# Kernel optimization log

Hardware: AMD Instinct MI355X
Metric: run time of the kernel (lower is better)

The kernel has to match this reference:

```python
import jax, jax.numpy as jnp
import numpy as np

SIZE = 2.0            # scene extent, matches init size
N_LEVELS = 16         # Instant-NGP default
TABLE_SIZE = 1 << 19  # hash entries per level (power of 2)
FEAT = 2              # embedding_length per level
BASE_RES = 16         # init resolution
MAX_RES = 2048
N_POINTS = 1 << 21

_OFFS = np.array([[(c >> d) & 1 for d in range(3)] for c in range(8)])  # [8,3] corner bits
_PRIMES = np.array([1, 2654435761, 805459861], dtype=np.uint32)         # NGP spatial hash primes


def setup_inputs() -> dict:
    key = jax.random.key(0)
    k1, k2 = jax.random.split(key)
    xyz = (jax.random.uniform(k1, (N_POINTS, 3), dtype=jnp.float32) - 0.5) * SIZE
    tables = jax.random.normal(k2, (N_LEVELS, TABLE_SIZE, FEAT), dtype=jnp.float32) * 1e-2
    # geometric resolution schedule 16 -> 2048 over 16 levels
    growth = (MAX_RES / BASE_RES) ** (np.arange(N_LEVELS) / (N_LEVELS - 1))
    resolutions = jnp.asarray(np.floor(BASE_RES * growth).astype(np.int32))
    return {"xyz": xyz, "tables": tables, "resolutions": resolutions}


def _encode(xyz, tables, resolutions):
    u = xyz / SIZE + 0.5                              # [N,3] in [0,1)
    offs_u = jnp.asarray(_OFFS.astype(np.uint32))     # [8,3]
    offs_f = jnp.asarray(_OFFS.astype(np.float32))    # [8,3]
    primes = jnp.asarray(_PRIMES)

    def level(_, xs):
        table, res = xs                               # [T,F], scalar int32
        p = u * res.astype(jnp.float32)               # [N,3]
        p0 = jnp.floor(p)
        w = p - p0                                    # trilinear fractions [N,3]
        c = p0.astype(jnp.uint32)[:, None, :] + offs_u[None]     # [N,8,3]
        h = (c[..., 0] * primes[0]) ^ (c[..., 1] * primes[1]) ^ (c[..., 2] * primes[2])
        idx = (h & jnp.uint32(TABLE_SIZE - 1)).astype(jnp.int32)  # [N,8]
        feats = table[idx]                                        # [N,8,F] gather
        wc = jnp.prod(jnp.where(offs_f[None] > 0, w[:, None, :], 1.0 - w[:, None, :]), axis=-1)  # [N,8]
        return None, jnp.sum(feats * wc[..., None], axis=1)      # [N,F]

    _, embs = jax.lax.scan(level, None, (tables, resolutions))   # [L,N,F]
    n = xyz.shape[0]
    return jnp.transpose(embs, (1, 0, 2)).reshape(n, N_LEVELS * FEAT)


def reference(xyz, tables, resolutions):
    return _encode(xyz, tables, resolutions)
```

## Files before the change

### kernel.cpp

```cpp
#include <hip/hip_runtime.h>
#include <hip/hip_fp16.h>

#define NLV 16
#define TBL (1u << 19)
#define TMASK (TBL - 1u)
#define P1 2654435761u
#define P2 805459861u

typedef float vf2 __attribute__((ext_vector_type(2)));
typedef float vf4 __attribute__((ext_vector_type(4)));
typedef unsigned vu2 __attribute__((ext_vector_type(2)));
typedef unsigned vu4 __attribute__((ext_vector_type(4)));

__device__ __forceinline__ vf2 h2_to_f2(unsigned bits) {
    union { unsigned u; __half2 h; } c; c.u = bits;
    float2 f = __half22float2(c.h);
    vf2 r; r.x = f.x; r.y = f.y; return r;
}
__device__ __forceinline__ unsigned f2_to_h2(float a, float b) {
    union { __half2 h; unsigned u; } c; c.h = __floats2half2_rn(a, b);
    return c.u;
}

__global__ __launch_bounds__(256) void convert_tables(
    const float* __restrict__ tables, unsigned* __restrict__ htab, int total)
{
    int i = blockIdx.x * 256 + threadIdx.x;
    int e0 = i * 2;
    if (e0 >= total) return;
    vf4 v = *(const vf4*)(tables + (size_t)e0 * 2);
    vu2 o; o.x = f2_to_h2(v.x, v.y); o.y = f2_to_h2(v.z, v.w);
    *(vu2*)(htab + e0) = o;
}

__global__ __launch_bounds__(256) void pack_u4(
    const float* __restrict__ xyz, vf4* __restrict__ u4, int n)
{
    int p = blockIdx.x * 256 + threadIdx.x;
    if (p >= n) return;
    float x = xyz[(size_t)p * 3 + 0];
    float y = xyz[(size_t)p * 3 + 1];
    float z = xyz[(size_t)p * 3 + 2];
    vf4 r; r.x = x * 0.5f + 0.5f; r.y = y * 0.5f + 0.5f;
    r.z = z * 0.5f + 0.5f; r.w = 0.0f;
    u4[p] = r;
}

__global__ __launch_bounds__(256) void ngp_gather_h(
    const vf4* __restrict__ u4,
    const unsigned* __restrict__ htab,
    const int* __restrict__ resolutions,
    unsigned* __restrict__ wsout,
    int n, int nbPerLevel)
{
    int L = blockIdx.x / nbPerLevel;
    int chunk = blockIdx.x % nbPerLevel;
    int p0 = chunk * 1024 + (int)threadIdx.x;

    float res = (float)resolutions[L];
    const unsigned* __restrict__ tab = htab + (size_t)L * TBL;
    unsigned* __restrict__ wl = wsout + (size_t)L * n;

    unsigned Rj[4][4];
    unsigned e[4], odd[4];
    float wx[4], wyz[4][4];
    bool valid[4];

#pragma unroll
    for (int q = 0; q < 4; ++q) {
        int p = p0 + q * 256;
        valid[q] = (p < n);
        int pp = valid[q] ? p : 0;
        vf4 u = u4[pp];
        float px = u.x * res, py = u.y * res, pz = u.z * res;
        float fx = floorf(px), fy = floorf(py), fz = floorf(pz);
        float wxl = px - fx, wyl = py - fy, wzl = pz - fz;
        unsigned cx = (unsigned)fx, cy = (unsigned)fy, cz = (unsigned)fz;
        e[q] = cx & ~1u;
        odd[q] = cx & 1u;
        unsigned hy0 = cy * P1, hy1 = hy0 + P1;
        unsigned hz0 = cz * P2, hz1 = hz0 + P2;
        Rj[q][0] = hy0 ^ hz0; Rj[q][1] = hy1 ^ hz0;
        Rj[q][2] = hy0 ^ hz1; Rj[q][3] = hy1 ^ hz1;
        float vy = 1.0f - wyl, vz = 1.0f - wzl;
        wx[q] = wxl;
        wyz[q][0] = vy * vz; wyz[q][1] = wyl * vz;
        wyz[q][2] = vy * wzl; wyz[q][3] = wyl * wzl;
    }

    vu2 dA[4][4];
#pragma unroll
    for (int q = 0; q < 4; ++q)
#pragma unroll
        for (int j = 0; j < 4; ++j) {
            unsigned idx = (e[q] ^ Rj[q][j]) & TMASK;
            dA[q][j] = *(const vu2*)(tab + (idx & ~1u));
        }

    vu2 dB[4][4];
#pragma unroll
    for (int q = 0; q < 4; ++q) {
#pragma unroll
        for (int j = 0; j < 4; ++j) { dB[q][j].x = 0u; dB[q][j].y = 0u; }
        if (odd[q]) {
#pragma unroll
            for (int j = 0; j < 4; ++j) {
                unsigned idx = ((e[q] + 2u) ^ Rj[q][j]) & TMASK;
                dB[q][j] = *(const vu2*)(tab + (idx & ~1u));
            }
        }
    }

#pragma unroll
    for (int q = 0; q < 4; ++q) {
        float vx = 1.0f - wx[q];
        float a0 = 0.0f, a1 = 0.0f;
#pragma unroll
        for (int j = 0; j < 4; ++j) {
            unsigned sA = Rj[q][j] & 1u;
            unsigned s0 = sA ^ odd[q];
            unsigned b0 = s0 ? dA[q][j].y : dA[q][j].x;
            unsigned fromA = sA ? dA[q][j].x : dA[q][j].y;
            unsigned fromB = sA ? dB[q][j].y : dB[q][j].x;
            unsigned b1 = odd[q] ? fromB : fromA;
            vf2 f0 = h2_to_f2(b0);
            vf2 f1 = h2_to_f2(b1);
            float W0 = wyz[q][j] * vx;
            float W1 = wyz[q][j] * wx[q];
            a0 += f0.x * W0; a0 += f1.x * W1;
            a1 += f0.y * W0; a1 += f1.y * W1;
        }
        int p = p0 + q * 256;
        if (valid[q]) wl[p] = f2_to_h2(a0, a1);
    }
}

__global__ __launch_bounds__(256) void ngp_transpose_h(
    const unsigned* __restrict__ ws,
    float* __restrict__ out, int n)
{
    int t = blockIdx.x * 256 + threadIdx.x;
    int p = t * 4;
    if (p >= n) return;

    if (p + 3 < n && (n & 3) == 0) {
        vu4 m[NLV];
#pragma unroll
        for (int L = 0; L < NLV; ++L)
            m[L] = *(const vu4*)(ws + (size_t)L * n + p);
#pragma unroll
        for (int pt = 0; pt < 4; ++pt) {
            vf4* o = (vf4*)(out + (size_t)(p + pt) * (NLV * 2));
#pragma unroll
            for (int i = 0; i < 8; ++i) {
                unsigned ba = pt == 0 ? m[2 * i].x : pt == 1 ? m[2 * i].y
                             : pt == 2 ? m[2 * i].z : m[2 * i].w;
                unsigned bb = pt == 0 ? m[2 * i + 1].x : pt == 1 ? m[2 * i + 1].y
                             : pt == 2 ? m[2 * i + 1].z : m[2 * i + 1].w;
                vf2 ga = h2_to_f2(ba), gb = h2_to_f2(bb);
                vf4 r; r.x = ga.x; r.y = ga.y; r.z = gb.x; r.w = gb.y;
                o[i] = r;
            }
        }
    } else {
        for (int pt = 0; pt < 4 && p + pt < n; ++pt) {
            vf4* o = (vf4*)(out + (size_t)(p + pt) * (NLV * 2));
#pragma unroll
            for (int i = 0; i < 8; ++i) {
                vf2 ga = h2_to_f2(ws[(size_t)(2 * i) * n + p + pt]);
                vf2 gb = h2_to_f2(ws[(size_t)(2 * i + 1) * n + p + pt]);
                vf4 r; r.x = ga.x; r.y = ga.y; r.z = gb.x; r.w = gb.y;
                o[i] = r;
            }
        }
    }
}

__global__ __launch_bounds__(256) void ngp_encode_kernel(
    const float* __restrict__ xyz,
    const float* __restrict__ tables,
    const int* __restrict__ resolutions,
    float* __restrict__ out,
    int n)
{
    int p = blockIdx.x * blockDim.x + threadIdx.x;
    if (p >= n) return;

    float x = xyz[(size_t)p * 3 + 0];
    float y = xyz[(size_t)p * 3 + 1];
    float z = xyz[(size_t)p * 3 + 2];
    float ux = x * 0.5f + 0.5f;
    float uy = y * 0.5f + 0.5f;
    float uz = z * 0.5f + 0.5f;

    float acc[NLV * 2];

#pragma unroll
    for (int L = 0; L < NLV; ++L) {
        float res = (float)resolutions[L];
        float px = ux * res, py = uy * res, pz = uz * res;
        float fx = floorf(px), fy = floorf(py), fz = floorf(pz);
        float wx = px - fx, wy = py - fy, wz = pz - fz;
        unsigned cx = (unsigned)fx, cy = (unsigned)fy, cz = (unsigned)fz;
        unsigned hx0 = cx, hx1 = cx + 1u;
        unsigned hy0 = cy * P1, hy1 = hy0 + P1;
        unsigned hz0 = cz * P2, hz1 = hz0 + P2;
        const vf2* __restrict__ tab = (const vf2*)tables + (size_t)L * TBL;
        float vx = 1.0f - wx, vy = 1.0f - wy, vz = 1.0f - wz;
        float a0 = 0.0f, a1 = 0.0f;
#pragma unroll
        for (int c = 0; c < 8; ++c) {
            unsigned h = ((c & 1) ? hx1 : hx0) ^
                         ((c & 2) ? hy1 : hy0) ^
                         ((c & 4) ? hz1 : hz0);
            vf2 f = tab[h & TMASK];
            float w = ((c & 1) ? wx : vx) *
                      ((c & 2) ? wy : vy) *
                      ((c & 4) ? wz : vz);
            a0 += f.x * w;
            a1 += f.y * w;
        }
        acc[L * 2 + 0] = a0;
        acc[L * 2 + 1] = a1;
    }

    vf4* o = (vf4*)(out + (size_t)p * (NLV * 2));
#pragma unroll
    for (int i = 0; i < 8; ++i) {
        vf4 r; r.x = acc[i * 4 + 0]; r.y = acc[i * 4 + 1];
        r.z = acc[i * 4 + 2]; r.w = acc[i * 4 + 3];
        o[i] = r;
    }
}

extern "C" void kernel_launch(void* const* d_in, const int* in_sizes, int n_in,
                              void* d_out, int out_size, void* d_ws, size_t ws_size,
                              hipStream_t stream) {
    const float* xyz = (const float*)d_in[0];
    const float* tables = (const float*)d_in[1];
    const int* resolutions = (const int*)d_in[2];
    float* out = (float*)d_out;

    int n = in_sizes[0] / 3;
    const int totalEntries = NLV * (int)TBL;
    const size_t tabBytes = (size_t)totalEntries * 4;
    const size_t u4Bytes = (size_t)n * sizeof(vf4);
    const size_t wsoutBytes = (size_t)NLV * (size_t)n * 4;

    if (ws_size >= tabBytes + u4Bytes + wsoutBytes) {
        unsigned* htab = (unsigned*)d_ws;
        vf4* u4 = (vf4*)((char*)d_ws + tabBytes);
        unsigned* wsout = (unsigned*)((char*)d_ws + tabBytes + u4Bytes);

        int gridC = (totalEntries / 2 + 255) / 256;
        hipLaunchKernelGGL(convert_tables, dim3(gridC), dim3(256), 0, stream,
                           tables, htab, totalEntries);

        int gridU = (n + 255) / 256;
        hipLaunchKernelGGL(pack_u4, dim3(gridU), dim3(256), 0, stream,
                           xyz, u4, n);

        int nbPerLevel = (n + 1023) / 1024;
        int grid1 = NLV * nbPerLevel;
        hipLaunchKernelGGL(ngp_gather_h, dim3(grid1), dim3(256), 0, stream,
                           u4, htab, resolutions, wsout, n, nbPerLevel);

        int grid2 = ((n + 3) / 4 + 255) / 256;
        hipLaunchKernelGGL(ngp_transpose_h, dim3(grid2), dim3(256), 0, stream,
                           wsout, out, n);
    } else {
        int grid = (n + 255) / 256;
        hipLaunchKernelGGL(ngp_encode_kernel, dim3(grid), dim3(256), 0, stream,
                           xyz, tables, resolutions, out, n);
    }
}
```

Baseline: 898.4 us.

## Sort points into Morton-ordered spatial bins before hash-grid gather

Adds a counting sort of points into 2^18 Morton-ordered spatial bins (histogram, single-block scan, atomic scatter), so the gather kernel processes spatially nearby points together and gets better cache locality in the hash tables. The gather now does eight plain 4-byte loads per point instead of the paired-entry trick, and the final kernel scatters rows back to original order through an index array. This costs three extra passes over the points, many atomics, and a serial one-block scan, and the final output writes become non-contiguous.

```diff
diff --git a/kernel.cpp b/kernel.cpp
--- a/kernel.cpp
+++ b/kernel.cpp
@@ -6,11 +6,11 @@
 #define TMASK (TBL - 1u)
 #define P1 2654435761u
 #define P2 805459861u
+#define NBIN (1 << 18)
 
 typedef float vf2 __attribute__((ext_vector_type(2)));
 typedef float vf4 __attribute__((ext_vector_type(4)));
 typedef unsigned vu2 __attribute__((ext_vector_type(2)));
-typedef unsigned vu4 __attribute__((ext_vector_type(4)));
 
 __device__ __forceinline__ vf2 h2_to_f2(unsigned bits) {
     union { unsigned u; __half2 h; } c; c.u = bits;
@@ -20,6 +20,22 @@
 __device__ __forceinline__ unsigned f2_to_h2(float a, float b) {
     union { __half2 h; unsigned u; } c; c.h = __floats2half2_rn(a, b);
     return c.u;
+}
+
+__device__ __forceinline__ unsigned mort6(unsigned v) {
+    v &= 63u;
+    v = (v | (v << 16)) & 0x030000FFu;
+    v = (v | (v << 8))  & 0x0300F00Fu;
+    v = (v | (v << 4))  & 0x030C30C3u;
+    v = (v | (v << 2))  & 0x09249249u;
+    return v;
+}
+
+__device__ __forceinline__ unsigned bin_of(float ux, float uy, float uz) {
+    unsigned bx = min(63u, (unsigned)(ux * 64.0f));
+    unsigned by = min(63u, (unsigned)(uy * 64.0f));
+    unsigned bz = min(63u, (unsigned)(uz * 64.0f));
+    return mort6(bx) | (mort6(by) << 1) | (mort6(bz) << 2);
 }
 
 __global__ __launch_bounds__(256) void convert_tables(
@@ -33,21 +49,57 @@
     *(vu2*)(htab + e0) = o;
 }
 
-__global__ __launch_bounds__(256) void pack_u4(
-    const float* __restrict__ xyz, vf4* __restrict__ u4, int n)
+__global__ __launch_bounds__(256) void hist_kernel(
+    const float* __restrict__ xyz, unsigned* __restrict__ hist, int n)
 {
     int p = blockIdx.x * 256 + threadIdx.x;
     if (p >= n) return;
-    float x = xyz[(size_t)p * 3 + 0];
-    float y = xyz[(size_t)p * 3 + 1];
-    float z = xyz[(size_t)p * 3 + 2];
-    vf4 r; r.x = x * 0.5f + 0.5f; r.y = y * 0.5f + 0.5f;
-    r.z = z * 0.5f + 0.5f; r.w = 0.0f;
-    u4[p] = r;
-}
-
-__global__ __launch_bounds__(256) void ngp_gather_h(
-    const vf4* __restrict__ u4,
+    float ux = xyz[(size_t)p * 3 + 0] * 0.5f + 0.5f;
+    float uy = xyz[(size_t)p * 3 + 1] * 0.5f + 0.5f;
+    float uz = xyz[(size_t)p * 3 + 2] * 0.5f + 0.5f;
+    atomicAdd(&hist[bin_of(ux, uy, uz)], 1u);
+}
+
+__global__ __launch_bounds__(1024) void scan_bins(unsigned* __restrict__ hist)
+{
+    __shared__ unsigned part[1024];
+    int t = threadIdx.x;
+    int base = t * (NBIN / 1024);
+    unsigned s = 0;
+    for (int j = 0; j < NBIN / 1024; ++j) s += hist[base + j];
+    part[t] = s;
+    __syncthreads();
+    for (int off = 1; off < 1024; off <<= 1) {
+        unsigned v = (t >= off) ? part[t - off] : 0u;
+        __syncthreads();
+        part[t] += v;
+        __syncthreads();
+    }
+    unsigned run = (t == 0) ? 0u : part[t - 1];
+    for (int j = 0; j < NBIN / 1024; ++j) {
+        unsigned tmp = hist[base + j];
+        hist[base + j] = run;
+        run += tmp;
+    }
+}
+
+__global__ __launch_bounds__(256) void scatter_kernel(
+    const float* __restrict__ xyz, unsigned* __restrict__ start,
+    vf4* __restrict__ u4s, int* __restrict__ orig, int n)
+{
+    int p = blockIdx.x * 256 + threadIdx.x;
+    if (p >= n) return;
+    float ux = xyz[(size_t)p * 3 + 0] * 0.5f + 0.5f;
+    float uy = xyz[(size_t)p * 3 + 1] * 0.5f + 0.5f;
+    float uz = xyz[(size_t)p * 3 + 2] * 0.5f + 0.5f;
+    unsigned pos = atomicAdd(&start[bin_of(ux, uy, uz)], 1u);
+    orig[pos] = p;
+    vf4 r; r.x = ux; r.y = uy; r.z = uz; r.w = 0.0f;
+    u4s[pos] = r;
+}
+
+__global__ __launch_bounds__(256) void ngp_gather_s(
+    const vf4* __restrict__ u4s,
     const unsigned* __restrict__ htab,
     const int* __restrict__ resolutions,
     unsigned* __restrict__ wsout,
@@ -61,8 +113,7 @@
     const unsigned* __restrict__ tab = htab + (size_t)L * TBL;
     unsigned* __restrict__ wl = wsout + (size_t)L * n;
 
-    unsigned Rj[4][4];
-    unsigned e[4], odd[4];
+    unsigned idx[4][8];
     float wx[4], wyz[4][4];
     bool valid[4];
 
@@ -71,108 +122,62 @@
         int p = p0 + q * 256;
         valid[q] = (p < n);
         int pp = valid[q] ? p : 0;
-        vf4 u = u4[pp];
+        vf4 u = u4s[pp];
         float px = u.x * res, py = u.y * res, pz = u.z * res;
         float fx = floorf(px), fy = floorf(py), fz = floorf(pz);
         float wxl = px - fx, wyl = py - fy, wzl = pz - fz;
         unsigned cx = (unsigned)fx, cy = (unsigned)fy, cz = (unsigned)fz;
-        e[q] = cx & ~1u;
-        odd[q] = cx & 1u;
+        unsigned hx0 = cx, hx1 = cx + 1u;
         unsigned hy0 = cy * P1, hy1 = hy0 + P1;
         unsigned hz0 = cz * P2, hz1 = hz0 + P2;
-        Rj[q][0] = hy0 ^ hz0; Rj[q][1] = hy1 ^ hz0;
-        Rj[q][2] = hy0 ^ hz1; Rj[q][3] = hy1 ^ hz1;
+#pragma unroll
+        for (int c = 0; c < 8; ++c)
+            idx[q][c] = ((((c & 1) ? hx1 : hx0) ^
+                          ((c & 2) ? hy1 : hy0) ^
+                          ((c & 4) ? hz1 : hz0)) & TMASK);
         float vy = 1.0f - wyl, vz = 1.0f - wzl;
         wx[q] = wxl;
-        wyz[q][0] = vy * vz; wyz[q][1] = wyl * vz;
+        wyz[q][0] = vy * vz;  wyz[q][1] = wyl * vz;
         wyz[q][2] = vy * wzl; wyz[q][3] = wyl * wzl;
     }
 
-    vu2 dA[4][4];
+    unsigned d[4][8];
 #pragma unroll
     for (int q = 0; q < 4; ++q)
 #pragma unroll
-        for (int j = 0; j < 4; ++j) {
-            unsigned idx = (e[q] ^ Rj[q][j]) & TMASK;
-            dA[q][j] = *(const vu2*)(tab + (idx & ~1u));
-        }
-
-    vu2 dB[4][4];
-#pragma unroll
-    for (int q = 0; q < 4; ++q) {
-#pragma unroll
-        for (int j = 0; j < 4; ++j) { dB[q][j].x = 0u; dB[q][j].y = 0u; }
-        if (odd[q]) {
-#pragma unroll
-            for (int j = 0; j < 4; ++j) {
-                unsigned idx = ((e[q] + 2u) ^ Rj[q][j]) & TMASK;
-                dB[q][j] = *(const vu2*)(tab + (idx & ~1u));
-            }
-        }
-    }
+        for (int c = 0; c < 8; ++c)
+            d[q][c] = tab[idx[q][c]];
 
 #pragma unroll
     for (int q = 0; q < 4; ++q) {
         float vx = 1.0f - wx[q];
         float a0 = 0.0f, a1 = 0.0f;
 #pragma unroll
-        for (int j = 0; j < 4; ++j) {
-            unsigned sA = Rj[q][j] & 1u;
-            unsigned s0 = sA ^ odd[q];
-            unsigned b0 = s0 ? dA[q][j].y : dA[q][j].x;
-            unsigned fromA = sA ? dA[q][j].x : dA[q][j].y;
-            unsigned fromB = sA ? dB[q][j].y : dB[q][j].x;
-            unsigned b1 = odd[q] ? fromB : fromA;
-            vf2 f0 = h2_to_f2(b0);
-            vf2 f1 = h2_to_f2(b1);
-            float W0 = wyz[q][j] * vx;
-            float W1 = wyz[q][j] * wx[q];
-            a0 += f0.x * W0; a0 += f1.x * W1;
-            a1 += f0.y * W0; a1 += f1.y * W1;
+        for (int c = 0; c < 8; ++c) {
+            float w = wyz[q][c >> 1] * ((c & 1) ? wx[q] : vx);
+            vf2 f = h2_to_f2(d[q][c]);
+            a0 += f.x * w;
+            a1 += f.y * w;
         }
         int p = p0 + q * 256;
         if (valid[q]) wl[p] = f2_to_h2(a0, a1);
     }
 }
 
-__global__ __launch_bounds__(256) void ngp_transpose_h(
-    const unsigned* __restrict__ ws,
+__global__ __launch_bounds__(256) void ngp_finalize_s(
+    const unsigned* __restrict__ ws, const int* __restrict__ orig,
     float* __restrict__ out, int n)
 {
-    int t = blockIdx.x * 256 + threadIdx.x;
-    int p = t * 4;
-    if (p >= n) return;
-
-    if (p + 3 < n && (n & 3) == 0) {
-        vu4 m[NLV];
-#pragma unroll
-        for (int L = 0; L < NLV; ++L)
-            m[L] = *(const vu4*)(ws + (size_t)L * n + p);
-#pragma unroll
-        for (int pt = 0; pt < 4; ++pt) {
-            vf4* o = (vf4*)(out + (size_t)(p + pt) * (NLV * 2));
-#pragma unroll
-            for (int i = 0; i < 8; ++i) {
-                unsigned ba = pt == 0 ? m[2 * i].x : pt == 1 ? m[2 * i].y
-                             : pt == 2 ? m[2 * i].z : m[2 * i].w;
-                unsigned bb = pt == 0 ? m[2 * i + 1].x : pt == 1 ? m[2 * i + 1].y
-                             : pt == 2 ? m[2 * i + 1].z : m[2 * i + 1].w;
-                vf2 ga = h2_to_f2(ba), gb = h2_to_f2(bb);
-                vf4 r; r.x = ga.x; r.y = ga.y; r.z = gb.x; r.w = gb.y;
-                o[i] = r;
-            }
-        }
-    } else {
-        for (int pt = 0; pt < 4 && p + pt < n; ++pt) {
-            vf4* o = (vf4*)(out + (size_t)(p + pt) * (NLV * 2));
-#pragma unroll
-            for (int i = 0; i < 8; ++i) {
-                vf2 ga = h2_to_f2(ws[(size_t)(2 * i) * n + p + pt]);
-                vf2 gb = h2_to_f2(ws[(size_t)(2 * i + 1) * n + p + pt]);
-                vf4 r; r.x = ga.x; r.y = ga.y; r.z = gb.x; r.w = gb.y;
-                o[i] = r;
-            }
-        }
+    int i = blockIdx.x * 256 + threadIdx.x;
+    if (i >= n) return;
+    int op = orig[i];
+    vf4* o = (vf4*)(out + (size_t)op * (NLV * 2));
+#pragma unroll
+    for (int j = 0; j < 8; ++j) {
+        vf2 ga = h2_to_f2(ws[(size_t)(2 * j) * n + i]);
+        vf2 gb = h2_to_f2(ws[(size_t)(2 * j + 1) * n + i]);
+        vf4 r; r.x = ga.x; r.y = ga.y; r.z = gb.x; r.w = gb.y;
+        o[j] = r;
     }
 }
 
@@ -243,31 +248,42 @@
 
     int n = in_sizes[0] / 3;
     const int totalEntries = NLV * (int)TBL;
-    const size_t tabBytes = (size_t)totalEntries * 4;
-    const size_t u4Bytes = (size_t)n * sizeof(vf4);
+
+    const size_t tabBytes  = (size_t)totalEntries * 4;
+    const size_t u4Bytes   = (size_t)n * sizeof(vf4);
+    const size_t origBytes = (size_t)n * 4;
+    const size_t histBytes = (size_t)NBIN * 4;
     const size_t wsoutBytes = (size_t)NLV * (size_t)n * 4;
-
-    if (ws_size >= tabBytes + u4Bytes + wsoutBytes) {
-        unsigned* htab = (unsigned*)d_ws;
-        vf4* u4 = (vf4*)((char*)d_ws + tabBytes);
-        unsigned* wsout = (unsigned*)((char*)d_ws + tabBytes + u4Bytes);
+    const size_t need = tabBytes + u4Bytes + origBytes + histBytes + wsoutBytes;
+
+    if (ws_size >= need) {
+        char* base = (char*)d_ws;
+        unsigned* htab  = (unsigned*)base;                       base += tabBytes;
+        vf4*      u4s   = (vf4*)base;                            base += u4Bytes;
+        int*      orig  = (int*)base;                            base += origBytes;
+        unsigned* hist  = (unsigned*)base;                       base += histBytes;
+        unsigned* wsout = (unsigned*)base;
+
+        hipMemsetAsync(hist, 0, histBytes, stream);
 
         int gridC = (totalEntries / 2 + 255) / 256;
         hipLaunchKernelGGL(convert_tables, dim3(gridC), dim3(256), 0, stream,
                            tables, htab, totalEntries);
 
-        int gridU = (n + 255) / 256;
-        hipLaunchKernelGGL(pack_u4, dim3(gridU), dim3(256), 0, stream,
-                           xyz, u4, n);
+        int gridP = (n + 255) / 256;
+        hipLaunchKernelGGL(hist_kernel, dim3(gridP), dim3(256), 0, stream,
+                           xyz, hist, n);
+        hipLaunchKernelGGL(scan_bins, dim3(1), dim3(1024), 0, stream, hist);
+        hipLaunchKernelGGL(scatter_kernel, dim3(gridP), dim3(256), 0, stream,
+                           xyz, hist, u4s, orig, n);
 
         int nbPerLevel = (n + 1023) / 1024;
         int grid1 = NLV * nbPerLevel;
-        hipLaunchKernelGGL(ngp_gather_h, dim3(grid1), dim3(256), 0, stream,
-                           u4, htab, resolutions, wsout, n, nbPerLevel);
-
-        int grid2 = ((n + 3) / 4 + 255) / 256;
-        hipLaunchKernelGGL(ngp_transpose_h, dim3(grid2), dim3(256), 0, stream,
-                           wsout, out, n);
+        hipLaunchKernelGGL(ngp_gather_s, dim3(grid1), dim3(256), 0, stream,
+                           u4s, htab, resolutions, wsout, n, nbPerLevel);
+
+        hipLaunchKernelGGL(ngp_finalize_s, dim3(gridP), dim3(256), 0, stream,
+                           wsout, orig, out, n);
     } else {
         int grid = (n + 255) / 256;
         hipLaunchKernelGGL(ngp_encode_kernel, dim3(grid), dim3(256), 0, stream,
```

Result: no change. 884.2 us (-1.6%).
